# Optimization experiments

Hardware: AMD Instinct MI355X
Metric: run time of the kernel (lower is better)

The kernel has to match this reference:

```python
import jax, jax.numpy as jnp
import numpy as np
from jax import lax

STRIDE, PAD, DIL = 1, 1, 1  # main deform-conv hyperparams


def setup_inputs() -> dict:
    key = jax.random.key(0)
    k1, k2, k3, k4, k5 = jax.random.split(key, 5)
    B, C_in, C_out, L, K = 8, 256, 256, 4096, 3
    x = jax.random.normal(k1, (B, C_in, L), dtype=jnp.float32)
    # offset-field conv1d params (kernel 3, pad 1, produces C_in offset channels)
    offset_w = jax.random.normal(k2, (C_in, C_in, 3), dtype=jnp.float32) * 0.02
    offset_b = jax.random.normal(k3, (C_in,), dtype=jnp.float32) * 0.02
    # main deform conv params
    weight = jax.random.normal(k4, (C_out, C_in, K), dtype=jnp.float32) * 0.02
    bias = jax.random.normal(k5, (C_out,), dtype=jnp.float32) * 0.02
    return {"x": x, "offset_w": offset_w, "offset_b": offset_b, "weight": weight, "bias": bias}


def _deform_conv1d(x, offset_w, offset_b, weight, bias):
    B, C, L = x.shape
    K = weight.shape[-1]
    # offset field: Conv1d(C -> C, k=3, pad=1), one offset per channel per position
    off = lax.conv_general_dilated(
        x, offset_w, window_strides=(1,), padding=[(1, 1)],
        dimension_numbers=("NCH", "OIH", "NCH")) + offset_b[None, :, None]
    L_out = off.shape[-1]
    # base sampling grid: pos(k, p) = p*stride - pad + k*dil  -> [K, L_out]
    base = (jnp.arange(L_out, dtype=x.dtype) * STRIDE - PAD)[None, :] \
         + (jnp.arange(K, dtype=x.dtype) * DIL)[:, None]
    pos = base[None, None] + off[:, :, None, :]          # [B, C, K, L_out]
    p0 = jnp.floor(pos)
    w1 = pos - p0                                         # linear-interp weight
    i0 = p0.astype(jnp.int32)
    i1 = i0 + 1
    xb = jnp.broadcast_to(x[:, :, None, :], pos.shape)    # [B, C, K, L]
    g0 = jnp.take_along_axis(xb, jnp.clip(i0, 0, L - 1), axis=-1)
    g1 = jnp.take_along_axis(xb, jnp.clip(i1, 0, L - 1), axis=-1)
    zero = jnp.zeros((), x.dtype)
    v0 = jnp.where((i0 >= 0) & (i0 < L), g0, zero)
    v1 = jnp.where((i1 >= 0) & (i1 < L), g1, zero)
    sampled = v0 * (1 - w1) + v1 * w1                     # [B, C, K, L_out]
    out = jnp.einsum("ock,bckl->bol", weight, sampled) + bias[None, :, None]
    return out


def reference(x, offset_w, offset_b, weight, bias):
    return _deform_conv1d(x, offset_w, offset_b, weight, bias)
```

## Files before the change

kernel.cpp:

```cpp
#include <hip/hip_runtime.h>
#include <hip/hip_bf16.h>

#define B_  8
#define C_  256
#define L_  4096
#define KD_ 768
#define XPW 4112

typedef __attribute__((ext_vector_type(8))) __bf16 bf16x8;
typedef __attribute__((ext_vector_type(4))) float f32x4;
typedef __attribute__((ext_vector_type(8))) unsigned short u16x8;

__device__ __forceinline__ unsigned short f2bf(float f){
  union { float f; unsigned u; } v; v.f = f;
  unsigned r = v.u + 0x7fffu + ((v.u >> 16) & 1u);
  return (unsigned short)(r >> 16);
}
__device__ __forceinline__ float bf2f(unsigned short h){
  union { unsigned u; float f; } v; v.u = ((unsigned)h) << 16;
  return v.f;
}
__device__ __forceinline__ unsigned pk2bf(float lo, float hi){
  __hip_bfloat162 h2 = __float22bfloat162_rn(make_float2(lo, hi));
  unsigned u;
  __builtin_memcpy(&u, &h2, 4);
  return u;
}

__device__ __forceinline__ int swz(int row, int col){
  return (row << 7) + (col ^ ((row & 15) << 3));
}

__device__ __forceinline__ void stage_tile32k(const unsigned short* __restrict__ g,
                                              unsigned short* l, int t){
  int wid = t >> 6, lane = t & 63;
  #pragma unroll
  for (int s = 0; s < 4; ++s){
    int seg = wid * 4 + s;
    const char* src = (const char*)g + seg * 1024 + lane * 16;
    char* dst = (char*)l + seg * 1024;
    __builtin_amdgcn_global_load_lds(
        (const __attribute__((address_space(1))) unsigned int*)src,
        (__attribute__((address_space(3))) unsigned int*)dst, 16, 0, 0);
  }
}

__global__ __launch_bounds__(256) void prep(const float* __restrict__ offw,
                                            const float* __restrict__ w,
                                            const float* __restrict__ x,
                                            unsigned short* __restrict__ wO,
                                            unsigned short* __restrict__ wM,
                                            unsigned short* __restrict__ xpad){
  int blk = blockIdx.x;
  if (blk < 768){
    int idx = blk * 256 + threadIdx.x;
    int r = idx / KD_, rem = idx % KD_;
    int rt = r >> 7, row = r & 127;
    int ch = rem / 96, col = rem % 96;
    int pos = (rt * 8 + ch) * 16384 + swz(row, col);
    wO[pos] = f2bf(offw[idx]);
    wM[pos] = f2bf(w[idx]);
  } else {
    int row = blk - 768;
    const float4* src = reinterpret_cast<const float4*>(x + (size_t)row * L_);
    unsigned short* dr = xpad + (size_t)row * XPW;
    int tid = threadIdx.x;
    #pragma unroll
    for (int q = 0; q < 2; ++q){
      float4 f0 = src[tid * 4 + q * 2];
      float4 f1 = src[tid * 4 + q * 2 + 1];
      u16x8 h;
      h[0]=f2bf(f0.x); h[1]=f2bf(f0.y); h[2]=f2bf(f0.z); h[3]=f2bf(f0.w);
      h[4]=f2bf(f1.x); h[5]=f2bf(f1.y); h[6]=f2bf(f1.z); h[7]=f2bf(f1.w);
      *reinterpret_cast<u16x8*>(dr + 8 + tid * 16 + q * 8) = h;
    }
    if (tid < 2){
      u16x8 z = {};
      *reinterpret_cast<u16x8*>(dr + (tid == 0 ? 0 : 8 + L_)) = z;
    }
  }
}

template <int MODE, int PADDED>
__global__ __launch_bounds__(512, 4) void dconv_gemm(
    const void* __restrict__ xsrc,
    const unsigned short* __restrict__ wT,
    const float* __restrict__ bvec,
    const unsigned short* __restrict__ off_in,
    void* __restrict__ outp){
  __shared__ __align__(16) unsigned short As[16384];
  __shared__ __align__(16) unsigned short Bs[16384];

  int bid = blockIdx.x;
  int wk = (bid & 7) * 64 + (bid >> 3);
  int b  = wk >> 6;
  int yt = (wk >> 5) & 1;
  int lt = wk & 31;
  int l0 = lt * 128, m0 = yt * 128;

  int t = threadIdx.x, lane = t & 63, wid = t >> 6;
  int wm = wid >> 1, wn = wid & 1;
  const unsigned short* xbh = PADDED
      ? (const unsigned short*)xsrc + (size_t)b * C_ * XPW + 8
      : nullptr;
  const float* xbf = PADDED ? nullptr
      : (const float*)xsrc + (size_t)b * C_ * L_;
  const unsigned short* offp = off_in + (size_t)b * C_ * L_;
  const unsigned short* wBase = wT + (size_t)yt * 8 * 16384;
  f32x4 acc[2][4] = {};

  int lrow = t & 127;
  int l = l0 + lrow;
  int cphase = t >> 7;

  for (int ch = 0; ch < 8; ++ch){
    stage_tile32k(wBase + (size_t)ch * 16384, As, t);
    int cin = ch * 32;
    #pragma unroll
    for (int it = 0; it < 4; ++it){
      int ccp = it * 4 + cphase;
      int colb = ccp * 6;
      if (PADDED && !MODE){
        const unsigned short* xr0 = xbh + (size_t)(cin + ccp * 2) * XPW + (l - 1);
        const unsigned short* xr1 = xr0 + XPW;
        unsigned a0 = xr0[0], a1 = xr0[1], a2 = xr0[2];
        unsigned b0 = xr1[0], b1 = xr1[1], b2 = xr1[2];
        *reinterpret_cast<unsigned*>(&Bs[swz(lrow, colb    )]) = a0 | (a1 << 16);
        *reinterpret_cast<unsigned*>(&Bs[swz(lrow, colb + 2)]) = a2 | (b0 << 16);
        *reinterpret_cast<unsigned*>(&Bs[swz(lrow, colb + 4)]) = b1 | (b2 << 16);
      } else {
        float s[6];
        #pragma unroll
        for (int u = 0; u < 2; ++u){
          int c = cin + ccp * 2 + u;
          int i0; float w1;
          if (MODE){
            float off = bf2f(offp[(size_t)c * L_ + l]);
            float pos = (float)(l - 1) + off;
            if (PADDED) pos = fminf(fmaxf(pos, -6.f), (float)(L_ + 4));
            float p0 = floorf(pos);
            w1 = pos - p0; i0 = (int)p0;
          } else { i0 = l - 1; w1 = 0.f; }
          if (PADDED){
            const unsigned short* xr = xbh + (size_t)c * XPW + i0;
            float v0 = bf2f(xr[0]), v1 = bf2f(xr[1]), v2 = bf2f(xr[2]), v3 = bf2f(xr[3]);
            float w0 = 1.f - w1;
            s[u*3+0] = v0 * w0 + v1 * w1;
            s[u*3+1] = v1 * w0 + v2 * w1;
            s[u*3+2] = v2 * w0 + v3 * w1;
          } else {
            const float* xr = xbf + (size_t)c * L_;
            float v[4]; float w0 = 1.f - w1;
            #pragma unroll
            for (int j = 0; j < (MODE ? 4 : 3); ++j){
              int ix = i0 + j;
              v[j] = ((unsigned)ix < (unsigned)L_) ? xr[ix] : 0.f;
            }
            #pragma unroll
            for (int k = 0; k < 3; ++k)
              s[u*3+k] = MODE ? (v[k] * w0 + v[k+1] * w1) : v[k];
          }
        }
        #pragma unroll
        for (int q = 0; q < 3; ++q)
          *reinterpret_cast<unsigned*>(&Bs[swz(lrow, colb + 2*q)]) =
              pk2bf(s[2*q], s[2*q+1]);
      }
    }
    __syncthreads();
    #pragma unroll
    for (int kf = 0; kf < 3; ++kf){
      int col = kf * 32 + (lane >> 4) * 8;
      bf16x8 af[2], bfv[4];
      #pragma unroll
      for (int mi = 0; mi < 2; ++mi)
        af[mi] = __builtin_bit_cast(bf16x8,
          *reinterpret_cast<const u16x8*>(&As[swz(wm * 32 + mi * 16 + (lane & 15), col)]));
      #pragma unroll
      for (int ni = 0; ni < 4; ++ni)
        bfv[ni] = __builtin_bit_cast(bf16x8,
          *reinterpret_cast<const u16x8*>(&Bs[swz(wn * 64 + ni * 16 + (lane & 15), col)]));
      #pragma unroll
      for (int mi = 0; mi < 2; ++mi)
        #pragma unroll
        for (int ni = 0; ni < 4; ++ni)
          acc[mi][ni] = __builtin_amdgcn_mfma_f32_16x16x32_bf16(af[mi], bfv[ni], acc[mi][ni], 0, 0, 0);
    }
    __syncthreads();
  }

  int rg = lane >> 4, cx = lane & 15;
  if (MODE == 0){
    unsigned short* ob = (unsigned short*)outp + (size_t)b * C_ * L_;
    #pragma unroll
    for (int mi = 0; mi < 2; ++mi)
      #pragma unroll
      for (int r = 0; r < 4; ++r){
        int c = m0 + wm * 32 + mi * 16 + rg * 4 + r;
        float bv = bvec[c];
        #pragma unroll
        for (int ni = 0; ni < 4; ++ni){
          int ll = l0 + wn * 64 + ni * 16 + cx;
          ob[(size_t)c * L_ + ll] = f2bf(acc[mi][ni][r] + bv);
        }
      }
  } else {
    float* ob = (float*)outp + (size_t)b * C_ * L_;
    #pragma unroll
    for (int mi = 0; mi < 2; ++mi)
      #pragma unroll
      for (int r = 0; r < 4; ++r){
        int o = m0 + wm * 32 + mi * 16 + rg * 4 + r;
        float bv = bvec[o];
        #pragma unroll
        for (int ni = 0; ni < 4; ++ni){
          int ll = l0 + wn * 64 + ni * 16 + cx;
          ob[(size_t)o * L_ + ll] = acc[mi][ni][r] + bv;
        }
      }
  }
}

extern "C" void kernel_launch(void* const* d_in, const int* in_sizes, int n_in,
                              void* d_out, int out_size, void* d_ws, size_t ws_size,
                              hipStream_t stream){
  (void)in_sizes; (void)n_in; (void)out_size;
  const float* x   = (const float*)d_in[0];
  const float* ow  = (const float*)d_in[1];
  const float* obv = (const float*)d_in[2];
  const float* w   = (const float*)d_in[3];
  const float* bv  = (const float*)d_in[4];
  float* out = (float*)d_out;

  unsigned short* wO     = (unsigned short*)d_ws;
  unsigned short* wM     = wO + 2 * 8 * 16384;
  unsigned short* off_ws = wM + 2 * 8 * 16384;
  unsigned short* xpad   = off_ws + (size_t)B_ * C_ * L_;
  size_t need = (char*)(xpad + (size_t)B_ * C_ * XPW) - (char*)d_ws;
  bool pad_ok = ws_size >= need;

  prep<<<dim3(pad_ok ? 768 + 2048 : 768), dim3(256), 0, stream>>>(
      ow, w, x, wO, wM, xpad);
  dim3 blk(512), grd(512);
  if (pad_ok){
    dconv_gemm<0,1><<<grd, blk, 0, stream>>>(xpad, wO, obv, off_ws, off_ws);
    dconv_gemm<1,1><<<grd, blk, 0, stream>>>(xpad, wM, bv, off_ws, out);
  } else {
    dconv_gemm<0,0><<<grd, blk, 0, stream>>>(x, wO, obv, off_ws, off_ws);
    dconv_gemm<1,0><<<grd, blk, 0, stream>>>(x, wM, bv, off_ws, out);
  }
}
```

Measured before the change: 68.72 us.

## Halve block threads, enlarge per-warp MFMA tile, shrink LDS rows to 96 columns

The GEMM kernel now runs 256 threads per block instead of 512. Each warp computes a 64x64 output tile (4x4 MFMAs) instead of 32x64, so each warp reuses more fragments from LDS. LDS tiles drop the unused padding from 128 to 96 columns with a new XOR swizzle, which reduces shared memory to 48KB per block. Each thread also builds 4 channels' worth of B-tile data per iteration and writes it to LDS as 64-bit stores. The trade-off is higher register pressure from 16 accumulators per thread and fewer threads available for the gather-heavy B-tile build.

```diff
diff --git a/kernel.cpp b/kernel.cpp
--- a/kernel.cpp
+++ b/kernel.cpp
@@ -10,6 +10,7 @@
 typedef __attribute__((ext_vector_type(8))) __bf16 bf16x8;
 typedef __attribute__((ext_vector_type(4))) float f32x4;
 typedef __attribute__((ext_vector_type(8))) unsigned short u16x8;
+typedef __attribute__((ext_vector_type(2))) unsigned int u32x2;
 
 __device__ __forceinline__ unsigned short f2bf(float f){
   union { float f; unsigned u; } v; v.f = f;
@@ -27,16 +28,16 @@
   return u;
 }
 
-__device__ __forceinline__ int swz(int row, int col){
-  return (row << 7) + (col ^ ((row & 15) << 3));
-}
-
-__device__ __forceinline__ void stage_tile32k(const unsigned short* __restrict__ g,
+__device__ __forceinline__ int swz96(int row, int col){
+  return row * 96 + (col ^ (((row >> 2) & 3) << 3));
+}
+
+__device__ __forceinline__ void stage_tile24k(const unsigned short* __restrict__ g,
                                               unsigned short* l, int t){
   int wid = t >> 6, lane = t & 63;
   #pragma unroll
-  for (int s = 0; s < 4; ++s){
-    int seg = wid * 4 + s;
+  for (int s = 0; s < 6; ++s){
+    int seg = wid * 6 + s;
     const char* src = (const char*)g + seg * 1024 + lane * 16;
     char* dst = (char*)l + seg * 1024;
     __builtin_amdgcn_global_load_lds(
@@ -57,7 +58,7 @@
     int r = idx / KD_, rem = idx % KD_;
     int rt = r >> 7, row = r & 127;
     int ch = rem / 96, col = rem % 96;
-    int pos = (rt * 8 + ch) * 16384 + swz(row, col);
+    int pos = (rt * 8 + ch) * 12288 + swz96(row, col);
     wO[pos] = f2bf(offw[idx]);
     wM[pos] = f2bf(w[idx]);
   } else {
@@ -82,14 +83,14 @@
 }
 
 template <int MODE, int PADDED>
-__global__ __launch_bounds__(512, 4) void dconv_gemm(
+__global__ __launch_bounds__(256, 3) void dconv_gemm(
     const void* __restrict__ xsrc,
     const unsigned short* __restrict__ wT,
     const float* __restrict__ bvec,
     const unsigned short* __restrict__ off_in,
     void* __restrict__ outp){
-  __shared__ __align__(16) unsigned short As[16384];
-  __shared__ __align__(16) unsigned short Bs[16384];
+  __shared__ __align__(16) unsigned short As[12288];
+  __shared__ __align__(16) unsigned short Bs[12288];
 
   int bid = blockIdx.x;
   int wk = (bid & 7) * 64 + (bid >> 3);
@@ -106,33 +107,39 @@
   const float* xbf = PADDED ? nullptr
       : (const float*)xsrc + (size_t)b * C_ * L_;
   const unsigned short* offp = off_in + (size_t)b * C_ * L_;
-  const unsigned short* wBase = wT + (size_t)yt * 8 * 16384;
-  f32x4 acc[2][4] = {};
+  const unsigned short* wBase = wT + (size_t)yt * 8 * 12288;
+  f32x4 acc[4][4] = {};
 
   int lrow = t & 127;
   int l = l0 + lrow;
   int cphase = t >> 7;
 
   for (int ch = 0; ch < 8; ++ch){
-    stage_tile32k(wBase + (size_t)ch * 16384, As, t);
+    stage_tile24k(wBase + (size_t)ch * 12288, As, t);
     int cin = ch * 32;
     #pragma unroll
     for (int it = 0; it < 4; ++it){
-      int ccp = it * 4 + cphase;
-      int colb = ccp * 6;
+      int q = it * 2 + cphase;
+      int colb = q * 12;
       if (PADDED && !MODE){
-        const unsigned short* xr0 = xbh + (size_t)(cin + ccp * 2) * XPW + (l - 1);
-        const unsigned short* xr1 = xr0 + XPW;
-        unsigned a0 = xr0[0], a1 = xr0[1], a2 = xr0[2];
-        unsigned b0 = xr1[0], b1 = xr1[1], b2 = xr1[2];
-        *reinterpret_cast<unsigned*>(&Bs[swz(lrow, colb    )]) = a0 | (a1 << 16);
-        *reinterpret_cast<unsigned*>(&Bs[swz(lrow, colb + 2)]) = a2 | (b0 << 16);
-        *reinterpret_cast<unsigned*>(&Bs[swz(lrow, colb + 4)]) = b1 | (b2 << 16);
+        unsigned hv[12];
+        #pragma unroll
+        for (int u = 0; u < 4; ++u){
+          const unsigned short* xr = xbh + (size_t)(cin + q * 4 + u) * XPW + (l - 1);
+          hv[u*3+0] = xr[0]; hv[u*3+1] = xr[1]; hv[u*3+2] = xr[2];
+        }
+        #pragma unroll
+        for (int p = 0; p < 3; ++p){
+          u32x2 dw;
+          dw.x = hv[4*p+0] | (hv[4*p+1] << 16);
+          dw.y = hv[4*p+2] | (hv[4*p+3] << 16);
+          *reinterpret_cast<u32x2*>(&Bs[swz96(lrow, colb + p * 4)]) = dw;
+        }
       } else {
-        float s[6];
-        #pragma unroll
-        for (int u = 0; u < 2; ++u){
-          int c = cin + ccp * 2 + u;
+        float s[12];
+        #pragma unroll
+        for (int u = 0; u < 4; ++u){
+          int c = cin + q * 4 + u;
           int i0; float w1;
           if (MODE){
             float off = bf2f(offp[(size_t)c * L_ + l]);
@@ -141,20 +148,20 @@
             float p0 = floorf(pos);
             w1 = pos - p0; i0 = (int)p0;
           } else { i0 = l - 1; w1 = 0.f; }
+          float w0 = 1.f - w1;
           if (PADDED){
             const unsigned short* xr = xbh + (size_t)c * XPW + i0;
             float v0 = bf2f(xr[0]), v1 = bf2f(xr[1]), v2 = bf2f(xr[2]), v3 = bf2f(xr[3]);
-            float w0 = 1.f - w1;
             s[u*3+0] = v0 * w0 + v1 * w1;
             s[u*3+1] = v1 * w0 + v2 * w1;
             s[u*3+2] = v2 * w0 + v3 * w1;
           } else {
             const float* xr = xbf + (size_t)c * L_;
-            float v[4]; float w0 = 1.f - w1;
+            float v[4];
             #pragma unroll
-            for (int j = 0; j < (MODE ? 4 : 3); ++j){
+            for (int j = 0; j < 4; ++j){
               int ix = i0 + j;
-              v[j] = ((unsigned)ix < (unsigned)L_) ? xr[ix] : 0.f;
+              v[j] = (MODE || j < 3) && ((unsigned)ix < (unsigned)L_) ? xr[ix] : 0.f;
             }
             #pragma unroll
             for (int k = 0; k < 3; ++k)
@@ -162,26 +169,29 @@
           }
         }
         #pragma unroll
-        for (int q = 0; q < 3; ++q)
-          *reinterpret_cast<unsigned*>(&Bs[swz(lrow, colb + 2*q)]) =
-              pk2bf(s[2*q], s[2*q+1]);
+        for (int p = 0; p < 3; ++p){
+          u32x2 dw;
+          dw.x = pk2bf(s[4*p+0], s[4*p+1]);
+          dw.y = pk2bf(s[4*p+2], s[4*p+3]);
+          *reinterpret_cast<u32x2*>(&Bs[swz96(lrow, colb + p * 4)]) = dw;
+        }
       }
     }
     __syncthreads();
     #pragma unroll
     for (int kf = 0; kf < 3; ++kf){
       int col = kf * 32 + (lane >> 4) * 8;
-      bf16x8 af[2], bfv[4];
-      #pragma unroll
-      for (int mi = 0; mi < 2; ++mi)
+      bf16x8 af[4], bfv[4];
+      #pragma unroll
+      for (int mi = 0; mi < 4; ++mi)
         af[mi] = __builtin_bit_cast(bf16x8,
-          *reinterpret_cast<const u16x8*>(&As[swz(wm * 32 + mi * 16 + (lane & 15), col)]));
+          *reinterpret_cast<const u16x8*>(&As[swz96(wm * 64 + mi * 16 + (lane & 15), col)]));
       #pragma unroll
       for (int ni = 0; ni < 4; ++ni)
         bfv[ni] = __builtin_bit_cast(bf16x8,
-          *reinterpret_cast<const u16x8*>(&Bs[swz(wn * 64 + ni * 16 + (lane & 15), col)]));
-      #pragma unroll
-      for (int mi = 0; mi < 2; ++mi)
+          *reinterpret_cast<const u16x8*>(&Bs[swz96(wn * 64 + ni * 16 + (lane & 15), col)]));
+      #pragma unroll
+      for (int mi = 0; mi < 4; ++mi)
         #pragma unroll
         for (int ni = 0; ni < 4; ++ni)
           acc[mi][ni] = __builtin_amdgcn_mfma_f32_16x16x32_bf16(af[mi], bfv[ni], acc[mi][ni], 0, 0, 0);
@@ -193,10 +203,10 @@
   if (MODE == 0){
     unsigned short* ob = (unsigned short*)outp + (size_t)b * C_ * L_;
     #pragma unroll
-    for (int mi = 0; mi < 2; ++mi)
+    for (int mi = 0; mi < 4; ++mi)
       #pragma unroll
       for (int r = 0; r < 4; ++r){
-        int c = m0 + wm * 32 + mi * 16 + rg * 4 + r;
+        int c = m0 + wm * 64 + mi * 16 + rg * 4 + r;
         float bv = bvec[c];
         #pragma unroll
         for (int ni = 0; ni < 4; ++ni){
@@ -207,10 +217,10 @@
   } else {
     float* ob = (float*)outp + (size_t)b * C_ * L_;
     #pragma unroll
-    for (int mi = 0; mi < 2; ++mi)
+    for (int mi = 0; mi < 4; ++mi)
       #pragma unroll
       for (int r = 0; r < 4; ++r){
-        int o = m0 + wm * 32 + mi * 16 + rg * 4 + r;
+        int o = m0 + wm * 64 + mi * 16 + rg * 4 + r;
         float bv = bvec[o];
         #pragma unroll
         for (int ni = 0; ni < 4; ++ni){
@@ -233,15 +243,15 @@
   float* out = (float*)d_out;
 
   unsigned short* wO     = (unsigned short*)d_ws;
-  unsigned short* wM     = wO + 2 * 8 * 16384;
-  unsigned short* off_ws = wM + 2 * 8 * 16384;
+  unsigned short* wM     = wO + 2 * 8 * 12288;
+  unsigned short* off_ws = wM + 2 * 8 * 12288;
   unsigned short* xpad   = off_ws + (size_t)B_ * C_ * L_;
   size_t need = (char*)(xpad + (size_t)B_ * C_ * XPW) - (char*)d_ws;
   bool pad_ok = ws_size >= need;
 
   prep<<<dim3(pad_ok ? 768 + 2048 : 768), dim3(256), 0, stream>>>(
       ow, w, x, wO, wM, xpad);
-  dim3 blk(512), grd(512);
+  dim3 blk(256), grd(512);
   if (pad_ok){
     dconv_gemm<0,1><<<grd, blk, 0, stream>>>(xpad, wO, obv, off_ws, off_ws);
     dconv_gemm<1,1><<<grd, blk, 0, stream>>>(xpad, wM, bv, off_ws, out);
```

New measurement: 97.09 us. 41.3% more time.

## Fuse bf16 padded-x conversion into the offset-conv GEMM staging pass

Applied to the files above, without the earlier changes.

Removes the x-to-bf16 padded conversion from the prep kernel and instead has the first (offset) GEMM read fp32 x directly, build its B tile from it, and write the bf16 padded copy (center tap, only for the yt==0 half) plus zero pads as a side effect. This eliminates a separate pass over x and the dependency of the first GEMM on it. In exchange, the first GEMM reads fp32 with bounds checks instead of bf16, and adds scattered 2-byte global stores per element.

```diff
diff --git a/kernel.cpp b/kernel.cpp
--- a/kernel.cpp
+++ b/kernel.cpp
@@ -45,45 +45,23 @@
   }
 }
 
-__global__ __launch_bounds__(256) void prep(const float* __restrict__ offw,
-                                            const float* __restrict__ w,
-                                            const float* __restrict__ x,
-                                            unsigned short* __restrict__ wO,
-                                            unsigned short* __restrict__ wM,
-                                            unsigned short* __restrict__ xpad){
-  int blk = blockIdx.x;
-  if (blk < 768){
-    int idx = blk * 256 + threadIdx.x;
-    int r = idx / KD_, rem = idx % KD_;
-    int rt = r >> 7, row = r & 127;
-    int ch = rem / 96, col = rem % 96;
-    int pos = (rt * 8 + ch) * 16384 + swz(row, col);
-    wO[pos] = f2bf(offw[idx]);
-    wM[pos] = f2bf(w[idx]);
-  } else {
-    int row = blk - 768;
-    const float4* src = reinterpret_cast<const float4*>(x + (size_t)row * L_);
-    unsigned short* dr = xpad + (size_t)row * XPW;
-    int tid = threadIdx.x;
-    #pragma unroll
-    for (int q = 0; q < 2; ++q){
-      float4 f0 = src[tid * 4 + q * 2];
-      float4 f1 = src[tid * 4 + q * 2 + 1];
-      u16x8 h;
-      h[0]=f2bf(f0.x); h[1]=f2bf(f0.y); h[2]=f2bf(f0.z); h[3]=f2bf(f0.w);
-      h[4]=f2bf(f1.x); h[5]=f2bf(f1.y); h[6]=f2bf(f1.z); h[7]=f2bf(f1.w);
-      *reinterpret_cast<u16x8*>(dr + 8 + tid * 16 + q * 8) = h;
-    }
-    if (tid < 2){
-      u16x8 z = {};
-      *reinterpret_cast<u16x8*>(dr + (tid == 0 ? 0 : 8 + L_)) = z;
-    }
-  }
+__global__ __launch_bounds__(256) void prep_w(const float* __restrict__ offw,
+                                              const float* __restrict__ w,
+                                              unsigned short* __restrict__ wO,
+                                              unsigned short* __restrict__ wM){
+  int idx = blockIdx.x * 256 + threadIdx.x;
+  int r = idx / KD_, rem = idx % KD_;
+  int rt = r >> 7, row = r & 127;
+  int ch = rem / 96, col = rem % 96;
+  int pos = (rt * 8 + ch) * 16384 + swz(row, col);
+  wO[pos] = f2bf(offw[idx]);
+  wM[pos] = f2bf(w[idx]);
 }
 
 template <int MODE, int PADDED>
 __global__ __launch_bounds__(512, 4) void dconv_gemm(
-    const void* __restrict__ xsrc,
+    const float* __restrict__ x,
+    unsigned short* __restrict__ xpad,
     const unsigned short* __restrict__ wT,
     const float* __restrict__ bvec,
     const unsigned short* __restrict__ off_in,
@@ -100,11 +78,9 @@
 
   int t = threadIdx.x, lane = t & 63, wid = t >> 6;
   int wm = wid >> 1, wn = wid & 1;
-  const unsigned short* xbh = PADDED
-      ? (const unsigned short*)xsrc + (size_t)b * C_ * XPW + 8
-      : nullptr;
-  const float* xbf = PADDED ? nullptr
-      : (const float*)xsrc + (size_t)b * C_ * L_;
+  const float* xbf = x + (size_t)b * C_ * L_;
+  unsigned short* xpw = xpad + (size_t)b * C_ * XPW;
+  const unsigned short* xbh = xpad + (size_t)b * C_ * XPW + 8;
   const unsigned short* offp = off_in + (size_t)b * C_ * L_;
   const unsigned short* wBase = wT + (size_t)yt * 8 * 16384;
   f32x4 acc[2][4] = {};
@@ -120,28 +96,27 @@
     for (int it = 0; it < 4; ++it){
       int ccp = it * 4 + cphase;
       int colb = ccp * 6;
-      if (PADDED && !MODE){
-        const unsigned short* xr0 = xbh + (size_t)(cin + ccp * 2) * XPW + (l - 1);
-        const unsigned short* xr1 = xr0 + XPW;
-        unsigned a0 = xr0[0], a1 = xr0[1], a2 = xr0[2];
-        unsigned b0 = xr1[0], b1 = xr1[1], b2 = xr1[2];
-        *reinterpret_cast<unsigned*>(&Bs[swz(lrow, colb    )]) = a0 | (a1 << 16);
-        *reinterpret_cast<unsigned*>(&Bs[swz(lrow, colb + 2)]) = a2 | (b0 << 16);
-        *reinterpret_cast<unsigned*>(&Bs[swz(lrow, colb + 4)]) = b1 | (b2 << 16);
-      } else {
-        float s[6];
-        #pragma unroll
-        for (int u = 0; u < 2; ++u){
-          int c = cin + ccp * 2 + u;
+      float s[6];
+      #pragma unroll
+      for (int u = 0; u < 2; ++u){
+        int c = cin + ccp * 2 + u;
+        if (MODE == 0){
+          const float* xr = xbf + (size_t)c * L_;
+          #pragma unroll
+          for (int j = 0; j < 3; ++j){
+            int ix = l - 1 + j;
+            s[u*3+j] = ((unsigned)ix < (unsigned)L_) ? xr[ix] : 0.f;
+          }
+          if (PADDED)
+            if (yt == 0) xpw[(size_t)c * XPW + 8 + l] = f2bf(s[u*3+1]);
+        } else {
+          float off = bf2f(offp[(size_t)c * L_ + l]);
+          float pos = (float)(l - 1) + off;
           int i0; float w1;
-          if (MODE){
-            float off = bf2f(offp[(size_t)c * L_ + l]);
-            float pos = (float)(l - 1) + off;
-            if (PADDED) pos = fminf(fmaxf(pos, -6.f), (float)(L_ + 4));
+          if (PADDED){
+            pos = fminf(fmaxf(pos, -6.f), (float)(L_ + 4));
             float p0 = floorf(pos);
             w1 = pos - p0; i0 = (int)p0;
-          } else { i0 = l - 1; w1 = 0.f; }
-          if (PADDED){
             const unsigned short* xr = xbh + (size_t)c * XPW + i0;
             float v0 = bf2f(xr[0]), v1 = bf2f(xr[1]), v2 = bf2f(xr[2]), v3 = bf2f(xr[3]);
             float w0 = 1.f - w1;
@@ -149,23 +124,25 @@
             s[u*3+1] = v1 * w0 + v2 * w1;
             s[u*3+2] = v2 * w0 + v3 * w1;
           } else {
+            float p0 = floorf(pos);
+            w1 = pos - p0; i0 = (int)p0;
             const float* xr = xbf + (size_t)c * L_;
             float v[4]; float w0 = 1.f - w1;
             #pragma unroll
-            for (int j = 0; j < (MODE ? 4 : 3); ++j){
+            for (int j = 0; j < 4; ++j){
               int ix = i0 + j;
               v[j] = ((unsigned)ix < (unsigned)L_) ? xr[ix] : 0.f;
             }
             #pragma unroll
             for (int k = 0; k < 3; ++k)
-              s[u*3+k] = MODE ? (v[k] * w0 + v[k+1] * w1) : v[k];
+              s[u*3+k] = v[k] * w0 + v[k+1] * w1;
           }
         }
-        #pragma unroll
-        for (int q = 0; q < 3; ++q)
-          *reinterpret_cast<unsigned*>(&Bs[swz(lrow, colb + 2*q)]) =
-              pk2bf(s[2*q], s[2*q+1]);
       }
+      #pragma unroll
+      for (int q = 0; q < 3; ++q)
+        *reinterpret_cast<unsigned*>(&Bs[swz(lrow, colb + 2*q)]) =
+            pk2bf(s[2*q], s[2*q+1]);
     }
     __syncthreads();
     #pragma unroll
@@ -187,6 +164,17 @@
           acc[mi][ni] = __builtin_amdgcn_mfma_f32_16x16x32_bf16(af[mi], bfv[ni], acc[mi][ni], 0, 0, 0);
     }
     __syncthreads();
+  }
+
+  if (MODE == 0 && PADDED && yt == 0){
+    if (lt == 0 && t < 256){
+      u16x8 z = {};
+      *reinterpret_cast<u16x8*>(xpw + (size_t)t * XPW) = z;
+    }
+    if (lt == 31 && t < 256){
+      u16x8 z = {};
+      *reinterpret_cast<u16x8*>(xpw + (size_t)t * XPW + 8 + L_) = z;
+    }
   }
 
   int rg = lane >> 4, cx = lane & 15;
@@ -239,14 +227,13 @@
   size_t need = (char*)(xpad + (size_t)B_ * C_ * XPW) - (char*)d_ws;
   bool pad_ok = ws_size >= need;
 
-  prep<<<dim3(pad_ok ? 768 + 2048 : 768), dim3(256), 0, stream>>>(
-      ow, w, x, wO, wM, xpad);
+  prep_w<<<dim3(768), dim3(256), 0, stream>>>(ow, w, wO, wM);
   dim3 blk(512), grd(512);
   if (pad_ok){
-    dconv_gemm<0,1><<<grd, blk, 0, stream>>>(xpad, wO, obv, off_ws, off_ws);
-    dconv_gemm<1,1><<<grd, blk, 0, stream>>>(xpad, wM, bv, off_ws, out);
+    dconv_gemm<0,1><<<grd, blk, 0, stream>>>(x, xpad, wO, obv, off_ws, off_ws);
+    dconv_gemm<1,1><<<grd, blk, 0, stream>>>(x, xpad, wM, bv, off_ws, out);
   } else {
-    dconv_gemm<0,0><<<grd, blk, 0, stream>>>(x, wO, obv, off_ws, off_ws);
-    dconv_gemm<1,0><<<grd, blk, 0, stream>>>(x, wM, bv, off_ws, out);
-  }
-}
+    dconv_gemm<0,0><<<grd, blk, 0, stream>>>(x, xpad, wO, obv, off_ws, off_ws);
+    dconv_gemm<1,0><<<grd, blk, 0, stream>>>(x, xpad, wM, bv, off_ws, out);
+  }
+}
```

New measurement: 93.44 us. +36.0%, slower.
